# Performance work log

Measured on AMD Instinct MI355X. Metric: run time of the kernel, lower is better.

Reference implementation:

```python
import jax, jax.numpy as jnp
import numpy as np

LUT_DIM = 33  # standard 33^3 color LUT


def setup_inputs() -> dict:
    key = jax.random.key(0)
    k1, k2 = jax.random.split(key)
    # learned 3D LUT: [out_channels=3, D_b, D_g, D_r]
    lut = jax.random.normal(k1, (3, LUT_DIM, LUT_DIM, LUT_DIM), dtype=jnp.float32) * 0.1
    # input image batch in [0, 1): [B, 3, H, W]
    x = jax.random.uniform(k2, (4, 3, 1024, 1024), dtype=jnp.float32)
    return {"lut": lut, "x": x}


def reference(lut, x):
    """Trilinear interpolation of a 3D color LUT (image-adaptive-3DLUT forward).

    lut: [3, D, D, D] laid out as lut[c, ib, ig, ir] (flat index ir + ig*D + ib*D*D)
    x:   [B, 3, H, W] with channels (r, g, b) in [0, 1]
    returns: [B, 3, H, W]
    """
    dim = lut.shape[-1]
    scale = dim - 1  # 1 / binsize

    r, g, b = x[:, 0], x[:, 1], x[:, 2]  # each [B, H, W]

    def cell(c):
        s = c * scale
        idx = jnp.clip(jnp.floor(s), 0, scale - 1).astype(jnp.int32)
        return idx, s - idx.astype(s.dtype)  # integer cell, fractional offset

    ir, dr = cell(r)
    ig, dg = cell(g)
    ib, db = cell(b)

    lut_flat = lut.reshape(3, -1)  # [3, D^3], tiny and cache-resident

    out = jnp.zeros((3,) + r.shape, dtype=x.dtype)  # [3, B, H, W]
    # 8 corners of the enclosing LUT cell, trilinear weights
    for or_ in (0, 1):
        wr = dr if or_ else (1.0 - dr)
        for og in (0, 1):
            wg = dg if og else (1.0 - dg)
            for ob in (0, 1):
                wb = db if ob else (1.0 - db)
                flat = ((ib + ob) * dim + (ig + og)) * dim + (ir + or_)  # [B, H, W]
                corner = lut_flat[:, flat]  # gather -> [3, B, H, W]
                out = out + (wr * wg * wb)[None] * corner

    return jnp.transpose(out, (1, 0, 2, 3))  # [B, 3, H, W]
```

## Files before the change

kernel.cpp:

```cpp
#include <hip/hip_runtime.h>
#include <hip/hip_fp16.h>


#define LUT_D     33
#define LUT_DD    (LUT_D * LUT_D)
#define LUT_N     (LUT_D * LUT_D * LUT_D)
#define CH_STRIDE 35940
#define STAGE_G   (CH_STRIDE / 4)
#define HW4       (1024 * 1024 / 4)
#define NGROUPS   (4 * HW4)
#define NCHUNKS   256
#define THREADS   1024
#define ITERS     (NGROUPS / NCHUNKS / THREADS)

typedef float vfloat4 __attribute__((ext_vector_type(4)));

__device__ __forceinline__ unsigned int pack2(float a, float b) {
    union { __half2 h; unsigned int u; } cv;
    cv.h = __floats2half2_rn(a, b);
    return cv.u;
}
__device__ __forceinline__ float2 unpack2(unsigned int p) {
    union { unsigned int u; __half2 h; } cv;
    cv.u = p;
    return __half22float2(cv.h);
}

__global__ __launch_bounds__(256)
void lut_pack_kernel(const float* __restrict__ lut, unsigned int* __restrict__ W) {
    const int t = blockIdx.x * 256 + (int)threadIdx.x;
    if (t >= 3 * LUT_N) return;
    const int c = t / LUT_N;
    const int i = t - c * LUT_N;
    const float a = lut[t];
    const float b = (i + 1 < LUT_N) ? lut[t + 1] : 0.0f;
    W[c * CH_STRIDE + i] = pack2(a, b);
}

__global__ __launch_bounds__(THREADS)
void lut3d_trilerp_kernel(const unsigned int* __restrict__ W,
                          const float* __restrict__ x,
                          float* __restrict__ out) {
    extern __shared__ __align__(16) unsigned int P[];

    const int bx   = blockIdx.x;
    const int xcd  = bx & 7;
    const int c    = (bx >> 3) % 3;
    const int chunk = (bx / 24) * 8 + xcd;

    const unsigned int* src = W + c * CH_STRIDE;
    for (int s = 0; s < 9; ++s) {
        const int gid = s * THREADS + (int)threadIdx.x;
        if (gid < STAGE_G) {
            __builtin_amdgcn_global_load_lds(
                (const __attribute__((address_space(1))) void*)(src + gid * 4),
                (__attribute__((address_space(3))) void*)(P + gid * 4),
                16, 0, 0);
        }
    }
    __syncthreads();

    const float4* x4 = (const float4*)x;
    float4*       o4 = (float4*)out;

    const int g0 = chunk * (NGROUPS / NCHUNKS) + (int)threadIdx.x;

    float4 R[ITERS], G[ITERS], B[ITERS];
    int obase[ITERS];
#pragma unroll
    for (int it = 0; it < ITERS; ++it) {
        const int g     = g0 + it * THREADS;
        const int b_img = g >> 18;
        const int hw4   = g & (HW4 - 1);
        const int ibase = b_img * 3 * HW4 + hw4;
        R[it] = x4[ibase];
        G[it] = x4[ibase + HW4];
        B[it] = x4[ibase + 2 * HW4];
        obase[it] = ibase + c * HW4;
    }

#pragma unroll
    for (int it = 0; it < ITERS; ++it) {
        const float rr[4] = {R[it].x, R[it].y, R[it].z, R[it].w};
        const float gg[4] = {G[it].x, G[it].y, G[it].z, G[it].w};
        const float bb[4] = {B[it].x, B[it].y, B[it].z, B[it].w};

        int   idx[4];
        float dr[4], dg[4], db[4];
#pragma unroll
        for (int k = 0; k < 4; ++k) {
            const float sr = rr[k] * 32.0f;
            const float sg = gg[k] * 32.0f;
            const float sb = bb[k] * 32.0f;
            const float fr = fminf(fmaxf(floorf(sr), 0.0f), 31.0f);
            const float fg = fminf(fmaxf(floorf(sg), 0.0f), 31.0f);
            const float fb = fminf(fmaxf(floorf(sb), 0.0f), 31.0f);
            dr[k] = sr - fr;
            dg[k] = sg - fg;
            db[k] = sb - fb;
            idx[k] = ((int)fb * LUT_D + (int)fg) * LUT_D + (int)fr;
        }

        unsigned int q00[4], q01[4], q10[4], q11[4];
#pragma unroll
        for (int k = 0; k < 4; ++k) {
            q00[k] = P[idx[k]];
            q01[k] = P[idx[k] + LUT_D];
            q10[k] = P[idx[k] + LUT_DD];
            q11[k] = P[idx[k] + LUT_DD + LUT_D];
        }

        float oo[4];
#pragma unroll
        for (int k = 0; k < 4; ++k) {
            const float2 a00 = unpack2(q00[k]);
            const float2 a01 = unpack2(q01[k]);
            const float2 a10 = unpack2(q10[k]);
            const float2 a11 = unpack2(q11[k]);
            const float l00 = a00.x + dr[k] * (a00.y - a00.x);
            const float l01 = a01.x + dr[k] * (a01.y - a01.x);
            const float l10 = a10.x + dr[k] * (a10.y - a10.x);
            const float l11 = a11.x + dr[k] * (a11.y - a11.x);
            const float l0  = l00 + dg[k] * (l01 - l00);
            const float l1  = l10 + dg[k] * (l11 - l10);
            oo[k] = l0 + db[k] * (l1 - l0);
        }

        vfloat4 v = {oo[0], oo[1], oo[2], oo[3]};
        __builtin_nontemporal_store(v, (vfloat4*)&o4[obase[it]]);
    }
}

extern "C" void kernel_launch(void* const* d_in, const int* in_sizes, int n_in,
                              void* d_out, int out_size, void* d_ws, size_t ws_size,
                              hipStream_t stream) {
    const float*  lut = (const float*)d_in[0];
    const float*  x   = (const float*)d_in[1];
    float*        out = (float*)d_out;
    unsigned int* W   = (unsigned int*)d_ws;

    const int pack_grid = (3 * LUT_N + 255) / 256;
    lut_pack_kernel<<<pack_grid, 256, 0, stream>>>(lut, W);

    const int grid = 3 * NCHUNKS;
    const size_t lds_bytes = (size_t)STAGE_G * 16;
    lut3d_trilerp_kernel<<<grid, THREADS, lds_bytes, stream>>>(W, x, out);
}
```

Measured before the change: 117.0 us.

## Drop fp16 pair-packing prepass; stage raw fp32 LUT channel into LDS directly

Removes the separate LUT packing kernel that built half2 (value, next-value) pairs, and instead copies each channel's fp32 LUT slice straight into LDS with an alignment offset. Each pixel now does 8 scalar LDS reads instead of 4 packed reads, and fp16 rounding of LUT values goes away. This saves a kernel launch and the workspace round trip, but doubles LDS read traffic per pixel and adds more possible bank conflicts.

```diff
diff --git a/kernel.cpp b/kernel.cpp
--- a/kernel.cpp
+++ b/kernel.cpp
@@ -1,64 +1,49 @@
 #include <hip/hip_runtime.h>
-#include <hip/hip_fp16.h>
 
 
-#define LUT_D     33
-#define LUT_DD    (LUT_D * LUT_D)
-#define LUT_N     (LUT_D * LUT_D * LUT_D)
-#define CH_STRIDE 35940
-#define STAGE_G   (CH_STRIDE / 4)
-#define HW4       (1024 * 1024 / 4)
-#define NGROUPS   (4 * HW4)
-#define NCHUNKS   256
-#define THREADS   1024
-#define ITERS     (NGROUPS / NCHUNKS / THREADS)
+#define LUT_D      33
+#define LUT_DD     (LUT_D * LUT_D)
+#define LUT_N      (LUT_D * LUT_D * LUT_D)
+#define HW4        (1024 * 1024 / 4)
+#define NGROUPS    (4 * HW4)
+#define NCHUNKS    256
+#define THREADS    1024
+#define ITERS      (NGROUPS / NCHUNKS / THREADS)
+#define STAGE_FULL 8984
+#define LDS_FLOATS 35940
 
 typedef float vfloat4 __attribute__((ext_vector_type(4)));
 
-__device__ __forceinline__ unsigned int pack2(float a, float b) {
-    union { __half2 h; unsigned int u; } cv;
-    cv.h = __floats2half2_rn(a, b);
-    return cv.u;
-}
-__device__ __forceinline__ float2 unpack2(unsigned int p) {
-    union { unsigned int u; __half2 h; } cv;
-    cv.u = p;
-    return __half22float2(cv.h);
-}
-
-__global__ __launch_bounds__(256)
-void lut_pack_kernel(const float* __restrict__ lut, unsigned int* __restrict__ W) {
-    const int t = blockIdx.x * 256 + (int)threadIdx.x;
-    if (t >= 3 * LUT_N) return;
-    const int c = t / LUT_N;
-    const int i = t - c * LUT_N;
-    const float a = lut[t];
-    const float b = (i + 1 < LUT_N) ? lut[t + 1] : 0.0f;
-    W[c * CH_STRIDE + i] = pack2(a, b);
-}
-
 __global__ __launch_bounds__(THREADS)
-void lut3d_trilerp_kernel(const unsigned int* __restrict__ W,
+void lut3d_trilerp_kernel(const float* __restrict__ lut,
                           const float* __restrict__ x,
                           float* __restrict__ out) {
-    extern __shared__ __align__(16) unsigned int P[];
+    extern __shared__ __align__(16) float P[];
 
     const int bx   = blockIdx.x;
-    const int xcd  = bx & 7;
-    const int c    = (bx >> 3) % 3;
+    const int xcd   = bx & 7;
+    const int c     = (bx >> 3) % 3;
     const int chunk = (bx / 24) * 8 + xcd;
 
-    const unsigned int* src = W + c * CH_STRIDE;
+    const int f0  = c * LUT_N;
+    const int off = f0 & 3;
+    const float* ga = lut + (f0 - off);
+
     for (int s = 0; s < 9; ++s) {
         const int gid = s * THREADS + (int)threadIdx.x;
-        if (gid < STAGE_G) {
+        if (gid < STAGE_FULL) {
             __builtin_amdgcn_global_load_lds(
-                (const __attribute__((address_space(1))) void*)(src + gid * 4),
+                (const __attribute__((address_space(1))) void*)(ga + gid * 4),
                 (__attribute__((address_space(3))) void*)(P + gid * 4),
                 16, 0, 0);
         }
     }
+    if (threadIdx.x < 3) {
+        P[STAGE_FULL * 4 + threadIdx.x] = ga[STAGE_FULL * 4 + threadIdx.x];
+    }
     __syncthreads();
+
+    const float* L = P + off;
 
     const float4* x4 = (const float4*)x;
     float4*       o4 = (float4*)out;
@@ -101,26 +86,28 @@
             idx[k] = ((int)fb * LUT_D + (int)fg) * LUT_D + (int)fr;
         }
 
-        unsigned int q00[4], q01[4], q10[4], q11[4];
+        float c000[4], c001[4], c010[4], c011[4];
+        float c100[4], c101[4], c110[4], c111[4];
 #pragma unroll
         for (int k = 0; k < 4; ++k) {
-            q00[k] = P[idx[k]];
-            q01[k] = P[idx[k] + LUT_D];
-            q10[k] = P[idx[k] + LUT_DD];
-            q11[k] = P[idx[k] + LUT_DD + LUT_D];
+            const float* p = L + idx[k];
+            c000[k] = p[0];
+            c001[k] = p[1];
+            c010[k] = p[LUT_D];
+            c011[k] = p[LUT_D + 1];
+            c100[k] = p[LUT_DD];
+            c101[k] = p[LUT_DD + 1];
+            c110[k] = p[LUT_DD + LUT_D];
+            c111[k] = p[LUT_DD + LUT_D + 1];
         }
 
         float oo[4];
 #pragma unroll
         for (int k = 0; k < 4; ++k) {
-            const float2 a00 = unpack2(q00[k]);
-            const float2 a01 = unpack2(q01[k]);
-            const float2 a10 = unpack2(q10[k]);
-            const float2 a11 = unpack2(q11[k]);
-            const float l00 = a00.x + dr[k] * (a00.y - a00.x);
-            const float l01 = a01.x + dr[k] * (a01.y - a01.x);
-            const float l10 = a10.x + dr[k] * (a10.y - a10.x);
-            const float l11 = a11.x + dr[k] * (a11.y - a11.x);
+            const float l00 = c000[k] + dr[k] * (c001[k] - c000[k]);
+            const float l01 = c010[k] + dr[k] * (c011[k] - c010[k]);
+            const float l10 = c100[k] + dr[k] * (c101[k] - c100[k]);
+            const float l11 = c110[k] + dr[k] * (c111[k] - c110[k]);
             const float l0  = l00 + dg[k] * (l01 - l00);
             const float l1  = l10 + dg[k] * (l11 - l10);
             oo[k] = l0 + db[k] * (l1 - l0);
@@ -134,15 +121,12 @@
 extern "C" void kernel_launch(void* const* d_in, const int* in_sizes, int n_in,
                               void* d_out, int out_size, void* d_ws, size_t ws_size,
                               hipStream_t stream) {
-    const float*  lut = (const float*)d_in[0];
-    const float*  x   = (const float*)d_in[1];
-    float*        out = (float*)d_out;
-    unsigned int* W   = (unsigned int*)d_ws;
-
-    const int pack_grid = (3 * LUT_N + 255) / 256;
-    lut_pack_kernel<<<pack_grid, 256, 0, stream>>>(lut, W);
+    const float* lut = (const float*)d_in[0];
+    const float* x   = (const float*)d_in[1];
+    float*       out = (float*)d_out;
+    (void)d_ws; (void)ws_size;
 
     const int grid = 3 * NCHUNKS;
-    const size_t lds_bytes = (size_t)STAGE_G * 16;
-    lut3d_trilerp_kernel<<<grid, THREADS, lds_bytes, stream>>>(W, x, out);
+    const size_t lds_bytes = LDS_FLOATS * sizeof(float);
+    lut3d_trilerp_kernel<<<grid, THREADS, lds_bytes, stream>>>(lut, x, out);
 }
```

Result: no change. 117.1 us (+0.1%).

## Use persistent 256-block grid with double-buffered input loads and channel restaging

Applied to the files above, without the earlier changes.

The grid drops from 768 blocks to 256. Each block now walks a contiguous range of (channel, pixel-group) work, double-buffering its input loads in registers so the next step's loads overlap the current step's compute. The block restages the channel's LUT into LDS only when the channel changes. The LUT pairs are repacked along the b axis instead of r, which changes the LDS neighbour offsets and the interpolation order. This reduces LUT staging and launch overhead, at the cost of fewer blocks to hide latency and extra barriers at channel boundaries.

```diff
diff --git a/kernel.cpp b/kernel.cpp
--- a/kernel.cpp
+++ b/kernel.cpp
@@ -9,9 +9,10 @@
 #define STAGE_G   (CH_STRIDE / 4)
 #define HW4       (1024 * 1024 / 4)
 #define NGROUPS   (4 * HW4)
-#define NCHUNKS   256
 #define THREADS   1024
-#define ITERS     (NGROUPS / NCHUNKS / THREADS)
+#define GRID      256
+#define GPB       (3 * NGROUPS / GRID)
+#define STEPS     6
 
 typedef float vfloat4 __attribute__((ext_vector_type(4)));
 
@@ -33,65 +34,63 @@
     const int c = t / LUT_N;
     const int i = t - c * LUT_N;
     const float a = lut[t];
-    const float b = (i + 1 < LUT_N) ? lut[t + 1] : 0.0f;
+    const float b = (i + LUT_DD < LUT_N) ? lut[t + LUT_DD] : 0.0f;
     W[c * CH_STRIDE + i] = pack2(a, b);
 }
 
 __global__ __launch_bounds__(THREADS)
-void lut3d_trilerp_kernel(const unsigned int* __restrict__ W,
+void lut3d_trilerp_kernel(const unsigned int* __restrict__ Wsrc,
                           const float* __restrict__ x,
                           float* __restrict__ out) {
-    extern __shared__ __align__(16) unsigned int P[];
+    extern __shared__ __align__(16) unsigned int W[];
 
-    const int bx   = blockIdx.x;
-    const int xcd  = bx & 7;
-    const int c    = (bx >> 3) % 3;
-    const int chunk = (bx / 24) * 8 + xcd;
-
-    const unsigned int* src = W + c * CH_STRIDE;
-    for (int s = 0; s < 9; ++s) {
-        const int gid = s * THREADS + (int)threadIdx.x;
-        if (gid < STAGE_G) {
-            __builtin_amdgcn_global_load_lds(
-                (const __attribute__((address_space(1))) void*)(src + gid * 4),
-                (__attribute__((address_space(3))) void*)(P + gid * 4),
-                16, 0, 0);
-        }
-    }
-    __syncthreads();
+    const int t    = (int)threadIdx.x;
+    const int base = (int)blockIdx.x * GPB;
 
     const float4* x4 = (const float4*)x;
     float4*       o4 = (float4*)out;
 
-    const int g0 = chunk * (NGROUPS / NCHUNKS) + (int)threadIdx.x;
+    auto stage = [&](int c) {
+#pragma unroll
+        for (int s = 0; s < 9; ++s) {
+            const int gid = s * THREADS + t;
+            if (gid < STAGE_G) {
+                __builtin_amdgcn_global_load_lds(
+                    (const __attribute__((address_space(1))) void*)(Wsrc + c * CH_STRIDE + gid * 4),
+                    (__attribute__((address_space(3))) void*)(W + gid * 4),
+                    16, 0, 0);
+            }
+        }
+    };
 
-    float4 R[ITERS], G[ITERS], B[ITERS];
-    int obase[ITERS];
-#pragma unroll
-    for (int it = 0; it < ITERS; ++it) {
-        const int g     = g0 + it * THREADS;
-        const int b_img = g >> 18;
-        const int hw4   = g & (HW4 - 1);
-        const int ibase = b_img * 3 * HW4 + hw4;
-        R[it] = x4[ibase];
-        G[it] = x4[ibase + HW4];
-        B[it] = x4[ibase + 2 * HW4];
-        obase[it] = ibase + c * HW4;
-    }
+    float4 xR[2][2], xG[2][2], xB[2][2];
+    int    ibs[2][2];
 
-#pragma unroll
-    for (int it = 0; it < ITERS; ++it) {
-        const float rr[4] = {R[it].x, R[it].y, R[it].z, R[it].w};
-        const float gg[4] = {G[it].x, G[it].y, G[it].z, G[it].w};
-        const float bb[4] = {B[it].x, B[it].y, B[it].z, B[it].w};
+    auto loadg = [&](int s, int m, int p) {
+        const int gg  = base + s * 2048 + m * 1024 + t;
+        const int g   = gg & (NGROUPS - 1);
+        const int bi  = g >> 18;
+        const int hw4 = g & (HW4 - 1);
+        const int ib  = bi * 3 * HW4 + hw4;
+        ibs[p][m] = ib;
+        xR[p][m] = x4[ib];
+        xG[p][m] = x4[ib + HW4];
+        xB[p][m] = x4[ib + 2 * HW4];
+    };
+
+    auto dog = [&](int m, int p, int ch) {
+        const float4 R = xR[p][m], G = xG[p][m], B = xB[p][m];
+        const float rr[4] = {R.x, R.y, R.z, R.w};
+        const float gw[4] = {G.x, G.y, G.z, G.w};
+        const float bw[4] = {B.x, B.y, B.z, B.w};
 
         int   idx[4];
         float dr[4], dg[4], db[4];
 #pragma unroll
         for (int k = 0; k < 4; ++k) {
             const float sr = rr[k] * 32.0f;
-            const float sg = gg[k] * 32.0f;
-            const float sb = bb[k] * 32.0f;
+            const float sg = gw[k] * 32.0f;
+            const float sb = bw[k] * 32.0f;
             const float fr = fminf(fmaxf(floorf(sr), 0.0f), 31.0f);
             const float fg = fminf(fmaxf(floorf(sg), 0.0f), 31.0f);
             const float fb = fminf(fmaxf(floorf(sb), 0.0f), 31.0f);
@@ -104,30 +103,54 @@
         unsigned int q00[4], q01[4], q10[4], q11[4];
 #pragma unroll
         for (int k = 0; k < 4; ++k) {
-            q00[k] = P[idx[k]];
-            q01[k] = P[idx[k] + LUT_D];
-            q10[k] = P[idx[k] + LUT_DD];
-            q11[k] = P[idx[k] + LUT_DD + LUT_D];
+            q00[k] = W[idx[k]];
+            q01[k] = W[idx[k] + 1];
+            q10[k] = W[idx[k] + LUT_D];
+            q11[k] = W[idx[k] + LUT_D + 1];
         }
 
         float oo[4];
 #pragma unroll
         for (int k = 0; k < 4; ++k) {
-            const float2 a00 = unpack2(q00[k]);
-            const float2 a01 = unpack2(q01[k]);
-            const float2 a10 = unpack2(q10[k]);
-            const float2 a11 = unpack2(q11[k]);
-            const float l00 = a00.x + dr[k] * (a00.y - a00.x);
-            const float l01 = a01.x + dr[k] * (a01.y - a01.x);
-            const float l10 = a10.x + dr[k] * (a10.y - a10.x);
-            const float l11 = a11.x + dr[k] * (a11.y - a11.x);
-            const float l0  = l00 + dg[k] * (l01 - l00);
-            const float l1  = l10 + dg[k] * (l11 - l10);
-            oo[k] = l0 + db[k] * (l1 - l0);
+            const float2 a = unpack2(q00[k]);
+            const float2 b = unpack2(q01[k]);
+            const float2 c = unpack2(q10[k]);
+            const float2 d = unpack2(q11[k]);
+            const float v00 = a.x + db[k] * (a.y - a.x);
+            const float v01 = b.x + db[k] * (b.y - b.x);
+            const float v10 = c.x + db[k] * (c.y - c.x);
+            const float v11 = d.x + db[k] * (d.y - d.x);
+            const float v0  = v00 + dr[k] * (v01 - v00);
+            const float v1  = v10 + dr[k] * (v11 - v10);
+            oo[k] = v0 + dg[k] * (v1 - v0);
         }
+        vfloat4 v = {oo[0], oo[1], oo[2], oo[3]};
+        __builtin_nontemporal_store(v, (vfloat4*)&o4[ibs[p][m] + ch * HW4]);
+    };
 
-        vfloat4 v = {oo[0], oo[1], oo[2], oo[3]};
-        __builtin_nontemporal_store(v, (vfloat4*)&o4[obase[it]]);
+    int cur = base >> 20;
+    stage(cur);
+    loadg(0, 0, 0);
+    loadg(0, 1, 0);
+    __syncthreads();
+
+#pragma unroll
+    for (int s = 0; s < STEPS; ++s) {
+        const int p  = s & 1;
+        const int pn = p ^ 1;
+        const int ch = (base + s * 2048) >> 20;
+        if (ch != cur) {
+            __syncthreads();
+            stage(ch);
+            __syncthreads();
+            cur = ch;
+        }
+        if (s + 1 < STEPS) {
+            loadg(s + 1, 0, pn);
+            loadg(s + 1, 1, pn);
+        }
+        dog(0, p, ch);
+        dog(1, p, ch);
     }
 }
 
@@ -142,7 +165,6 @@
     const int pack_grid = (3 * LUT_N + 255) / 256;
     lut_pack_kernel<<<pack_grid, 256, 0, stream>>>(lut, W);
 
-    const int grid = 3 * NCHUNKS;
-    const size_t lds_bytes = (size_t)STAGE_G * 16;
-    lut3d_trilerp_kernel<<<grid, THREADS, lds_bytes, stream>>>(W, x, out);
+    const size_t lds_bytes = (size_t)CH_STRIDE * 4;
+    lut3d_trilerp_kernel<<<GRID, THREADS, lds_bytes, stream>>>(W, x, out);
 }
```

New measurement: 118.7 us. About the same (+1.5%).
